# Kernel optimization log

Hardware: AMD Instinct MI355X
Metric: run time of the kernel (lower is better)

Reference implementation:

```python
import jax, jax.numpy as jnp
import numpy as np

N_TERMS = 2048  # zonotope error terms (x[0] center + 2047 generators)
N = 4096        # neurons


def setup_inputs() -> dict:
    key = jax.random.key(0)
    x = jax.random.normal(key, (N_TERMS, N), dtype=jnp.float32)
    return {"x": x}


def reference(x):
    n_terms, n = x.shape
    # interval bounds of the zonotope
    abs_sum = jnp.sum(jnp.abs(x[1:]), axis=0)      # [n]
    upper = x[0] + abs_sum
    lower = x[0] - abs_sum

    cross = (lower * upper) < 0                    # neuron straddles 0
    pos = lower >= 0                               # strictly non-negative
    crossf = cross.astype(x.dtype)
    posf = pos.astype(x.dtype)

    # 'auto' lambda init: upper/(upper-lower) on crossing neurons, 1 on positive,
    # NaN (0/0) replaced by 0.5; lambda is set via .data => constant w.r.t. x.
    denom = upper - lower
    safe = denom != 0
    lam = posf + crossf * jnp.where(safe, upper / jnp.where(safe, denom, 1.0), 0.5)
    lam = jax.lax.stop_gradient(lam)

    delta = jnp.maximum(-lam * lower, (1.0 - lam) * upper)  # [n]

    center = (delta * 0.5 + lam * x[0]) * crossf + x[0] * posf
    gens = x[1:] * (lam * crossf + posf)                    # [n_terms-1, n]

    # Parallel stream-compaction: crossing neuron i gets its own new error row
    # at n_terms + (# crossings before i). Padded to worst case n new rows;
    # non-crossing writes land on distinct (row, col) slots with value 0.
    ci = cross.astype(jnp.int32)
    rows = n_terms + jnp.cumsum(ci) - ci               # exclusive prefix sum
    cols = jnp.arange(n)

    out = jnp.zeros((n_terms + n, n), x.dtype)
    out = out.at[0].set(center)
    out = out.at[1:n_terms].set(gens)
    out = out.at[rows, cols].add((delta * 0.5) * crossf)
    return out
```

## Files before the change

kernel.cpp:

```cpp
#include <hip/hip_runtime.h>

#define N_TERMS 2048
#define NCOL 4096
#define NC4 1024
#define NCHUNK 128
#define RPC (N_TERMS / NCHUNK)

typedef float f4_t __attribute__((ext_vector_type(4)));

__global__ void k_partial_abs(const float* __restrict__ x, float* __restrict__ partial) {
    int col4 = blockIdx.x * blockDim.x + threadIdx.x;
    int chunk = blockIdx.y;
    int r0 = chunk * RPC;
    int r1 = r0 + RPC;
    if (r0 == 0) r0 = 1;
    const f4_t* x4 = (const f4_t*)x;
    f4_t acc = {0.f, 0.f, 0.f, 0.f};
#pragma unroll
    for (int r = r0; r < r1; ++r) {
        f4_t v = x4[(long)r * NC4 + col4];
        acc.x += fabsf(v.x);
        acc.y += fabsf(v.y);
        acc.z += fabsf(v.z);
        acc.w += fabsf(v.w);
    }
    ((f4_t*)partial)[chunk * NC4 + col4] = acc;
}

__global__ void k_stats_zero(const float* __restrict__ x, const float* __restrict__ partial,
                             float* __restrict__ out, float* __restrict__ scale,
                             float* __restrict__ dhalf, int* __restrict__ crossflag) {
    const int b = blockIdx.x;
    const int t = threadIdx.x;

    if (b < 64) {
        const int lane = t & 63;
        const int q = t >> 6;
        const int c = b * 64 + lane;

        float s0 = 0.f, s1 = 0.f, s2 = 0.f, s3 = 0.f;
        const int k0 = q * 32;
#pragma unroll 8
        for (int k = 0; k < 32; k += 4) {
            s0 += partial[(k0 + k + 0) * NCOL + c];
            s1 += partial[(k0 + k + 1) * NCOL + c];
            s2 += partial[(k0 + k + 2) * NCOL + c];
            s3 += partial[(k0 + k + 3) * NCOL + c];
        }
        __shared__ float red[4][64];
        red[q][lane] = (s0 + s1) + (s2 + s3);
        __syncthreads();
        if (q == 0) {
            float s = (red[0][lane] + red[1][lane]) + (red[2][lane] + red[3][lane]);
            float x0 = x[c];
            float u = x0 + s;
            float l = x0 - s;
            bool cross = (l * u) < 0.0f;
            bool pos = (l >= 0.0f);
            float denom = u - l;
            float lam = (pos ? 1.0f : 0.0f) +
                        (cross ? ((denom != 0.0f) ? u / denom : 0.5f) : 0.0f);
            float delta = fmaxf(-lam * l, (1.0f - lam) * u);
            float crossf = cross ? 1.0f : 0.0f;
            float posf = pos ? 1.0f : 0.0f;
            out[c] = (delta * 0.5f + lam * x0) * crossf + x0 * posf;
            scale[c] = lam * crossf + posf;
            dhalf[c] = delta * 0.5f * crossf;
            crossflag[c] = cross ? 1 : 0;
        }
    } else {
        const int zb = b - 64;
        f4_t* o4 = (f4_t*)out;
        const long base4 = (long)N_TERMS * NC4 + (long)zb * 8192;
        const f4_t z = {0.f, 0.f, 0.f, 0.f};
#pragma unroll
        for (int i = 0; i < 32; ++i)
            __builtin_nontemporal_store(z, &o4[base4 + i * 256 + t]);
    }
}

__global__ void k_gens_scatter(const float* __restrict__ x, const float* __restrict__ scale,
                               const float* __restrict__ dhalf,
                               const int* __restrict__ crossflag,
                               float* __restrict__ out) {
    const int b = blockIdx.x;
    const int t = threadIdx.x;
    if (b < 2048) {
        const int g = b * 256 + t;
        const int col4 = g & 1023;
        const int group = g >> 10;
        const int r0 = group << 2;
        const f4_t* x4 = (const f4_t*)x;
        f4_t* o4 = (f4_t*)out;
        const f4_t sc = ((const f4_t*)scale)[col4];

        if (group == 0) {
#pragma unroll
            for (int r = 1; r < 4; ++r) {
                f4_t v = x4[(long)r * NC4 + col4] * sc;
                __builtin_nontemporal_store(v, &o4[(long)r * NC4 + col4]);
            }
        } else {
#pragma unroll
            for (int i = 0; i < 4; ++i) {
                const int r = r0 + i;
                f4_t v = x4[(long)r * NC4 + col4] * sc;
                __builtin_nontemporal_store(v, &o4[(long)r * NC4 + col4]);
            }
        }
    } else {
        const int T = 256;
        const int PER = NCOL / T;
        __shared__ int tsum[T];
        const int base = t * PER;
        int cf[PER];
        int ex[PER];
        int run = 0;
#pragma unroll
        for (int i = 0; i < PER; ++i) {
            cf[i] = crossflag[base + i];
            ex[i] = run;
            run += cf[i];
        }
        tsum[t] = run;
        __syncthreads();
        for (int off = 1; off < T; off <<= 1) {
            int v = 0;
            if (t >= off) v = tsum[t - off];
            __syncthreads();
            tsum[t] += v;
            __syncthreads();
        }
        const int excl = (t == 0) ? 0 : tsum[t - 1];
#pragma unroll
        for (int i = 0; i < PER; ++i) {
            if (cf[i]) {
                const int c = base + i;
                const long row = N_TERMS + excl + ex[i];
                out[row * (long)NCOL + c] = dhalf[c];
            }
        }
    }
}

extern "C" void kernel_launch(void* const* d_in, const int* in_sizes, int n_in,
                              void* d_out, int out_size, void* d_ws, size_t ws_size,
                              hipStream_t stream) {
    const float* x = (const float*)d_in[0];
    float* out = (float*)d_out;

    float* ws = (float*)d_ws;
    float* partial   = ws;
    float* scale     = partial + NCHUNK * NCOL;
    float* dhalf     = scale + NCOL;
    int*   crossflag = (int*)(dhalf + NCOL);

    k_partial_abs<<<dim3(NC4 / 256, NCHUNK), 256, 0, stream>>>(x, partial);
    k_stats_zero<<<576, 256, 0, stream>>>(x, partial, out, scale, dhalf, crossflag);
    k_gens_scatter<<<2049, 256, 0, stream>>>(x, scale, dhalf, crossflag, out);
}
```

Before: 137.1 us.

## Fuse stats, zeroing, gens and scatter into one kernel with atomic flags

Merges the stats/zero kernel and the gens/scatter kernel into a single launch. Zero-fill blocks and stats blocks signal completion through global atomic counters, and gens and scatter blocks spin-wait on those counters. Each gens block now handles two row groups, which halves the block count. The aim is to remove one kernel launch boundary and let the zero-fill overlap with the gens copy, at the cost of spin-waiting and a dependence on the scheduling order of blocks to avoid deadlock.

Result: slower. 244.3 us (+78.1%).

```diff
diff --git a/kernel.cpp b/kernel.cpp
--- a/kernel.cpp
+++ b/kernel.cpp
@@ -8,7 +8,12 @@
 
 typedef float f4_t __attribute__((ext_vector_type(4)));
 
-__global__ void k_partial_abs(const float* __restrict__ x, float* __restrict__ partial) {
+__global__ void k_partial_abs(const float* __restrict__ x, float* __restrict__ partial,
+                              int* __restrict__ ctrs) {
+    if (blockIdx.x == 0 && blockIdx.y == 0 && threadIdx.x == 0) {
+        ctrs[0] = 0;
+        ctrs[1] = 0;
+    }
     int col4 = blockIdx.x * blockDim.x + threadIdx.x;
     int chunk = blockIdx.y;
     int r0 = chunk * RPC;
@@ -27,16 +32,36 @@
     ((f4_t*)partial)[chunk * NC4 + col4] = acc;
 }
 
-__global__ void k_stats_zero(const float* __restrict__ x, const float* __restrict__ partial,
-                             float* __restrict__ out, float* __restrict__ scale,
-                             float* __restrict__ dhalf, int* __restrict__ crossflag) {
+__global__ __launch_bounds__(256) void k_main(
+    const float* __restrict__ x, const float* __restrict__ partial,
+    float* __restrict__ out, float* __restrict__ scale,
+    float* __restrict__ dhalf, int* __restrict__ crossflag,
+    int* __restrict__ ctrs) {
     const int b = blockIdx.x;
     const int t = threadIdx.x;
+    int* zdone = ctrs + 0;
+    int* sdone = ctrs + 1;
 
-    if (b < 64) {
+    __shared__ float red[4][64];
+    __shared__ int tsum[256];
+
+    if (b < 512) {
+        f4_t* o4 = (f4_t*)out;
+        const long base4 = (long)N_TERMS * NC4 + (long)b * 8192;
+        const f4_t z = {0.f, 0.f, 0.f, 0.f};
+#pragma unroll
+        for (int i = 0; i < 32; ++i)
+            __builtin_nontemporal_store(z, &o4[base4 + i * 256 + t]);
+        __syncthreads();
+        if (t == 0) {
+            __threadfence();
+            atomicAdd(zdone, 1);
+        }
+    } else if (b < 576) {
+        const int sb = b - 512;
         const int lane = t & 63;
         const int q = t >> 6;
-        const int c = b * 64 + lane;
+        const int c = sb * 64 + lane;
 
         float s0 = 0.f, s1 = 0.f, s2 = 0.f, s3 = 0.f;
         const int k0 = q * 32;
@@ -47,7 +72,6 @@
             s2 += partial[(k0 + k + 2) * NCOL + c];
             s3 += partial[(k0 + k + 3) * NCOL + c];
         }
-        __shared__ float red[4][64];
         red[q][lane] = (s0 + s1) + (s2 + s3);
         __syncthreads();
         if (q == 0) {
@@ -68,50 +92,59 @@
             dhalf[c] = delta * 0.5f * crossf;
             crossflag[c] = cross ? 1 : 0;
         }
-    } else {
-        const int zb = b - 64;
-        f4_t* o4 = (f4_t*)out;
-        const long base4 = (long)N_TERMS * NC4 + (long)zb * 8192;
-        const f4_t z = {0.f, 0.f, 0.f, 0.f};
-#pragma unroll
-        for (int i = 0; i < 32; ++i)
-            __builtin_nontemporal_store(z, &o4[base4 + i * 256 + t]);
-    }
-}
+        __syncthreads();
+        if (t == 0) {
+            __threadfence();
+            atomicAdd(sdone, 1);
+        }
+    } else if (b < 1600) {
+        if (t == 0) {
+            while (__hip_atomic_load(sdone, __ATOMIC_RELAXED,
+                                     __HIP_MEMORY_SCOPE_AGENT) < 64)
+                __builtin_amdgcn_s_sleep(8);
+        }
+        __syncthreads();
+        __threadfence();
 
-__global__ void k_gens_scatter(const float* __restrict__ x, const float* __restrict__ scale,
-                               const float* __restrict__ dhalf,
-                               const int* __restrict__ crossflag,
-                               float* __restrict__ out) {
-    const int b = blockIdx.x;
-    const int t = threadIdx.x;
-    if (b < 2048) {
-        const int g = b * 256 + t;
+        const int gb = b - 576;
+        const int g = gb * 256 + t;
         const int col4 = g & 1023;
-        const int group = g >> 10;
-        const int r0 = group << 2;
+        const int group0 = g >> 10;
         const f4_t* x4 = (const f4_t*)x;
         f4_t* o4 = (f4_t*)out;
         const f4_t sc = ((const f4_t*)scale)[col4];
-
-        if (group == 0) {
 #pragma unroll
-            for (int r = 1; r < 4; ++r) {
-                f4_t v = x4[(long)r * NC4 + col4] * sc;
-                __builtin_nontemporal_store(v, &o4[(long)r * NC4 + col4]);
-            }
-        } else {
+        for (int h = 0; h < 2; ++h) {
+            const int group = group0 + h * 256;
+            const int r0 = group << 2;
+            if (group == 0) {
 #pragma unroll
-            for (int i = 0; i < 4; ++i) {
-                const int r = r0 + i;
-                f4_t v = x4[(long)r * NC4 + col4] * sc;
-                __builtin_nontemporal_store(v, &o4[(long)r * NC4 + col4]);
+                for (int r = 1; r < 4; ++r) {
+                    f4_t v = x4[(long)r * NC4 + col4] * sc;
+                    __builtin_nontemporal_store(v, &o4[(long)r * NC4 + col4]);
+                }
+            } else {
+#pragma unroll
+                for (int i = 0; i < 4; ++i) {
+                    const int r = r0 + i;
+                    f4_t v = x4[(long)r * NC4 + col4] * sc;
+                    __builtin_nontemporal_store(v, &o4[(long)r * NC4 + col4]);
+                }
             }
         }
     } else {
+        if (t == 0) {
+            while (__hip_atomic_load(zdone, __ATOMIC_RELAXED,
+                                     __HIP_MEMORY_SCOPE_AGENT) < 512 ||
+                   __hip_atomic_load(sdone, __ATOMIC_RELAXED,
+                                     __HIP_MEMORY_SCOPE_AGENT) < 64)
+                __builtin_amdgcn_s_sleep(8);
+        }
+        __syncthreads();
+        __threadfence();
+
         const int T = 256;
         const int PER = NCOL / T;
-        __shared__ int tsum[T];
         const int base = t * PER;
         int cf[PER];
         int ex[PER];
@@ -154,8 +187,8 @@
     float* scale     = partial + NCHUNK * NCOL;
     float* dhalf     = scale + NCOL;
     int*   crossflag = (int*)(dhalf + NCOL);
+    int*   ctrs      = crossflag + NCOL;
 
-    k_partial_abs<<<dim3(NC4 / 256, NCHUNK), 256, 0, stream>>>(x, partial);
-    k_stats_zero<<<576, 256, 0, stream>>>(x, partial, out, scale, dhalf, crossflag);
-    k_gens_scatter<<<2049, 256, 0, stream>>>(x, scale, dhalf, crossflag, out);
+    k_partial_abs<<<dim3(NC4 / 256, NCHUNK), 256, 0, stream>>>(x, partial, ctrs);
+    k_main<<<1601, 256, 0, stream>>>(x, partial, out, scale, dhalf, crossflag, ctrs);
 }
```
